# Kernel tuning notes

Measured on AMD Instinct MI355X. Metric: run time of the kernel, lower is better.

The kernel has to match this reference:

```python
import jax, jax.numpy as jnp
import numpy as np

BATCH = 4096
DIM = 2048
TEMPERATURE = 0.5


def setup_inputs() -> dict:
    key = jax.random.key(0)
    k1, k2 = jax.random.split(key)
    c_i = jax.random.normal(k1, (BATCH, DIM), dtype=jnp.float32)
    c_j = jax.random.normal(k2, (BATCH, DIM), dtype=jnp.float32)
    return {"c_i": c_i, "c_j": c_j}


def reference(c_i, c_j):
    # Original torch loop computes, for each i,j:
    #   kl[i, j] = sum_k softmax(c_j[j])_k * (log_softmax(c_j[j])_k - log_softmax(c_i[i])_k)
    #   logits = -kl / T ; loss = CE(logits, arange(B), reduction='sum') / B
    # Fused: kl = hneg[None, :] - Li @ Q.T where hneg[j] = sum_k Q[j]*logQ[j].
    B = c_i.shape[0]
    Li = jax.nn.log_softmax(c_i, axis=-1)          # [B, D]
    LQ = jax.nn.log_softmax(c_j, axis=-1)          # [B, D]
    Q = jnp.exp(LQ)                                # softmax(c_j)
    hneg = jnp.sum(Q * LQ, axis=-1)                # [B] negative entropy of each c_j row
    cross = jnp.einsum("id,jd->ij", Li, Q)         # [B, B] sum_k Li[i,k]*Q[j,k]
    kl = hneg[None, :] - cross                     # [B, B]
    logits = -kl / TEMPERATURE
    logp = jax.nn.log_softmax(logits, axis=-1)     # [B, B]
    loss = -jnp.sum(jnp.diagonal(logp)) / B        # CE(sum) / batch_size
    return loss
```

## Files before the change

### kernel.cpp

```cpp
#include <hip/hip_runtime.h>
#include <hip/hip_bf16.h>
#include <math.h>

#define BATCH 4096
#define DIM   2048
#define INV_T 2.0f

#define BM 128
#define BN 128

typedef float floatx4 __attribute__((ext_vector_type(4)));
typedef int   intx4   __attribute__((ext_vector_type(4)));
typedef int   intx8   __attribute__((ext_vector_type(8)));

static __device__ __forceinline__ void gld_lds16(const void* g, void* l) {
  __builtin_amdgcn_global_load_lds(
      (const __attribute__((address_space(1))) void*)g,
      (__attribute__((address_space(3))) void*)l, 16, 0, 0);
}

static __device__ __forceinline__ intx8 comb8(intx4 lo, intx4 hi) {
  intx8 r;
  r[0] = lo[0]; r[1] = lo[1]; r[2] = lo[2]; r[3] = lo[3];
  r[4] = hi[0]; r[5] = hi[1]; r[6] = hi[2]; r[7] = hi[3];
  return r;
}

__global__ __launch_bounds__(256) void prep_kernel(
    const float* __restrict__ ci, const float* __restrict__ cj,
    unsigned char* __restrict__ Li8, unsigned char* __restrict__ Qb8,
    float* __restrict__ hneg, float* __restrict__ isc,
    float* __restrict__ rowsum, float* __restrict__ out)
{
  const int lane = threadIdx.x & 63;
  const int wave = threadIdx.x >> 6;
  const int row = blockIdx.x * 4 + wave;
  const bool isj = row >= BATCH;
  const int r = isj ? row - BATCH : row;
  const float* __restrict__ src = (isj ? cj : ci) + (size_t)r * DIM;

  float v[32];
  #pragma unroll
  for (int i = 0; i < 8; ++i) {
    float4 t = ((const float4*)src)[i * 64 + lane];
    v[i * 4 + 0] = t.x; v[i * 4 + 1] = t.y;
    v[i * 4 + 2] = t.z; v[i * 4 + 3] = t.w;
  }

  float m = v[0];
  #pragma unroll
  for (int i = 1; i < 32; ++i) m = fmaxf(m, v[i]);
  #pragma unroll
  for (int off = 32; off >= 1; off >>= 1) m = fmaxf(m, __shfl_xor(m, off));

  float s = 0.f;
  #pragma unroll
  for (int i = 0; i < 32; ++i) s += __expf(v[i] - m);
  #pragma unroll
  for (int off = 32; off >= 1; off >>= 1) s += __shfl_xor(s, off);
  const float ls = m + __logf(s);

  float scale = 1.f;
  int t = 0;
  if (isj) {
    const float qmax = __expf(m - ls);
    const int be = (int)((__float_as_uint(qmax) >> 23) & 0xff);
    t = 134 - be;
    scale = __uint_as_float((unsigned)(t + 127) << 23);
  }

  unsigned char* dst = (isj ? Qb8 : Li8) + (size_t)r * DIM;
  float h = 0.f;
  #pragma unroll
  for (int i = 0; i < 8; ++i) {
    float f[4];
    #pragma unroll
    for (int j = 0; j < 4; ++j) {
      const float li = v[i * 4 + j] - ls;
      if (isj) {
        const float q = __expf(li);
        h += q * li;
        f[j] = q * scale;
      } else {
        f[j] = li;
      }
    }
    int w = __builtin_amdgcn_cvt_pk_fp8_f32(f[0], f[1], 0, false);
    w = __builtin_amdgcn_cvt_pk_fp8_f32(f[2], f[3], w, true);
    ((int*)dst)[i * 64 + lane] = w;
  }

  if (isj) {
    #pragma unroll
    for (int off = 32; off >= 1; off >>= 1) h += __shfl_xor(h, off);
    if (lane == 0) {
      hneg[r] = h;
      isc[r] = __uint_as_float((unsigned)(127 - t) << 23);
      rowsum[r] = 0.f;
    }
  }
  if (row == 0 && lane == 0) out[0] = 0.f;
}

__global__ __launch_bounds__(256, 3) void gemm_lse_kernel(
    const unsigned char* __restrict__ Li8, const unsigned char* __restrict__ Qb8,
    const float* __restrict__ hneg, const float* __restrict__ isc,
    float* __restrict__ rowsum, float* __restrict__ diag)
{
  __shared__ __attribute__((aligned(16))) unsigned char As[BM * 128];
  __shared__ __attribute__((aligned(16))) unsigned char Bs[BN * 128];

  const int tid  = threadIdx.x;
  const int lin = blockIdx.x;
  const int xc  = lin & 7;
  const int sq  = lin >> 3;
  const int bx  = (xc << 2) | (sq & 3);
  const int by  = sq >> 2;
  const int lane = tid & 63;
  const int wave = tid >> 6;
  const int wm   = (wave >> 1) * 64;
  const int wn   = (wave & 1) * 64;

  int soff[4];
  #pragma unroll
  for (int s = 0; s < 4; ++s) {
    const int p = tid + 256 * s;
    const int row = p >> 3;
    const int cbg = (p & 7) ^ (row & 7);
    soff[s] = row * DIM + cbg * 16;
  }
  const unsigned char* Abase = Li8 + (size_t)(by * BM) * DIM;
  const unsigned char* Bbase = Qb8 + (size_t)(bx * BN) * DIM;

  const int rl = lane & 15;
  const int q  = lane >> 4;
  const int sw = rl & 7;

  floatx4 acc[4][4];
  const floatx4 z = {0.f, 0.f, 0.f, 0.f};
  #pragma unroll
  for (int mt = 0; mt < 4; ++mt)
    #pragma unroll
    for (int nt = 0; nt < 4; ++nt) acc[mt][nt] = z;

  for (int k = 0; k < DIM; k += 128) {
    #pragma unroll
    for (int s = 0; s < 4; ++s) {
      gld_lds16(Abase + soff[s] + k, As + (tid + 256 * s) * 16);
      gld_lds16(Bbase + soff[s] + k, Bs + (tid + 256 * s) * 16);
    }
    __syncthreads();

    intx8 bf[4];
    #pragma unroll
    for (int t = 0; t < 4; ++t) {
      const int rb = wn + t * 16 + rl;
      const int q0 = rb * 8 + ((2 * q) ^ sw);
      const int q1 = rb * 8 + ((2 * q + 1) ^ sw);
      bf[t] = comb8(*(const intx4*)(Bs + q0 * 16), *(const intx4*)(Bs + q1 * 16));
    }
    #pragma unroll
    for (int mt = 0; mt < 4; ++mt) {
      const int ra = wm + mt * 16 + rl;
      const int p0 = ra * 8 + ((2 * q) ^ sw);
      const int p1 = ra * 8 + ((2 * q + 1) ^ sw);
      const intx8 af = comb8(*(const intx4*)(As + p0 * 16),
                             *(const intx4*)(As + p1 * 16));
      #pragma unroll
      for (int nt = 0; nt < 4; ++nt)
        acc[mt][nt] = __builtin_amdgcn_mfma_scale_f32_16x16x128_f8f6f4(
            af, bf[nt], acc[mt][nt],
            0, 0,
            0, 127,
            0, 127);
    }
    __syncthreads();
  }

  const int col0 = bx * BN + wn + rl;
  float hn[4], sc[4];
  #pragma unroll
  for (int nt = 0; nt < 4; ++nt) {
    hn[nt] = hneg[col0 + nt * 16];
    sc[nt] = isc[col0 + nt * 16];
  }
  const int row0 = by * BM + wm + (q << 2);

  if (bx == by && wm == wn && q == (rl >> 2)) {
    #pragma unroll
    for (int mt = 0; mt < 4; ++mt)
      diag[by * BM + wm + mt * 16 + rl] = acc[mt][mt][rl & 3] * sc[mt];
  }

  #pragma unroll
  for (int mt = 0; mt < 4; ++mt) {
    #pragma unroll
    for (int rr = 0; rr < 4; ++rr) {
      float p = 0.f;
      #pragma unroll
      for (int nt = 0; nt < 4; ++nt)
        p += __expf(INV_T * (acc[mt][nt][rr] * sc[nt] - hn[nt]));
      p += __shfl_xor(p, 1);
      p += __shfl_xor(p, 2);
      p += __shfl_xor(p, 4);
      p += __shfl_xor(p, 8);
      if (rl == 0)
        atomicAdd(&rowsum[row0 + mt * 16 + rr], p);
    }
  }
}

__global__ __launch_bounds__(256) void finalize_kernel(
    const float* __restrict__ hneg, const float* __restrict__ rowsum,
    const float* __restrict__ diag, float* __restrict__ out)
{
  const int i = blockIdx.x * 256 + threadIdx.x;
  const int lane = threadIdx.x & 63;
  const int wave = threadIdx.x >> 6;

  float c = __logf(rowsum[i]) - INV_T * (diag[i] - hneg[i]);
  #pragma unroll
  for (int off = 32; off >= 1; off >>= 1) c += __shfl_xor(c, off);

  __shared__ float red[4];
  if (lane == 0) red[wave] = c;
  __syncthreads();
  if (threadIdx.x == 0)
    atomicAdd(out, (red[0] + red[1] + red[2] + red[3]) * (1.0f / BATCH));
}

extern "C" void kernel_launch(void* const* d_in, const int* in_sizes, int n_in,
                              void* d_out, int out_size, void* d_ws, size_t ws_size,
                              hipStream_t stream) {
  const float* ci = (const float*)d_in[0];
  const float* cj = (const float*)d_in[1];
  float* out = (float*)d_out;

  unsigned char* Li8 = (unsigned char*)d_ws;
  unsigned char* Qb8 = Li8 + (size_t)BATCH * DIM;
  float* hneg   = (float*)(Qb8 + (size_t)BATCH * DIM);
  float* isc    = hneg + BATCH;
  float* rowsum = isc + BATCH;
  float* diag   = rowsum + BATCH;

  prep_kernel<<<2 * BATCH / 4, 256, 0, stream>>>(ci, cj, Li8, Qb8, hneg, isc, rowsum, out);
  gemm_lse_kernel<<<(BATCH / BM) * (BATCH / BN), 256, 0, stream>>>(Li8, Qb8, hneg, isc, rowsum, diag);
  finalize_kernel<<<BATCH / 256, 256, 0, stream>>>(hneg, rowsum, diag, out);
}
```

Measured before the change: 148.6 us.

## Enlarge GEMM tiles to 256x256 with double-buffered LDS prefetch pipeline

Grows the block tile from 128x128 to 256x256 with 512 threads (8 waves, each computing 128x64). LDS is double-buffered so the next K-slice's global-to-LDS loads are issued in phases and overlap the MFMAs, with manual waitcnt/barriers and setprio around the MFMA bursts. This is meant to cut global traffic per FLOP and hide load latency. In exchange it raises LDS use to 128KB per block and register pressure, which lowers occupancy, and leaves only 256 blocks for the grid.

```diff
diff --git a/kernel.cpp b/kernel.cpp
--- a/kernel.cpp
+++ b/kernel.cpp
@@ -6,8 +6,8 @@
 #define DIM   2048
 #define INV_T 2.0f
 
-#define BM 128
-#define BN 128
+#define BM 256
+#define BN 256
 
 typedef float floatx4 __attribute__((ext_vector_type(4)));
 typedef int   intx4   __attribute__((ext_vector_type(4)));
@@ -102,29 +102,30 @@
   if (row == 0 && lane == 0) out[0] = 0.f;
 }
 
-__global__ __launch_bounds__(256, 3) void gemm_lse_kernel(
+__global__ __launch_bounds__(512, 2) void gemm_lse_kernel(
     const unsigned char* __restrict__ Li8, const unsigned char* __restrict__ Qb8,
     const float* __restrict__ hneg, const float* __restrict__ isc,
     float* __restrict__ rowsum, float* __restrict__ diag)
 {
-  __shared__ __attribute__((aligned(16))) unsigned char As[BM * 128];
-  __shared__ __attribute__((aligned(16))) unsigned char Bs[BN * 128];
+  __shared__ __attribute__((aligned(16))) unsigned char As_[2][BM * 128];
+  __shared__ __attribute__((aligned(16))) unsigned char Bs_[2][BN * 128];
 
   const int tid  = threadIdx.x;
   const int lin = blockIdx.x;
   const int xc  = lin & 7;
   const int sq  = lin >> 3;
-  const int bx  = (xc << 2) | (sq & 3);
-  const int by  = sq >> 2;
+  const int by  = (xc & 3) * 4 + (sq & 3);
+  const int bx  = (xc >> 2) * 8 + (sq >> 2);
+
   const int lane = tid & 63;
   const int wave = tid >> 6;
-  const int wm   = (wave >> 1) * 64;
-  const int wn   = (wave & 1) * 64;
+  const int wm   = wave >> 2;
+  const int wn   = wave & 3;
 
   int soff[4];
   #pragma unroll
   for (int s = 0; s < 4; ++s) {
-    const int p = tid + 256 * s;
+    const int p = tid + 512 * s;
     const int row = p >> 3;
     const int cbg = (p & 7) ^ (row & 7);
     soff[s] = row * DIM + cbg * 16;
@@ -136,64 +137,106 @@
   const int q  = lane >> 4;
   const int sw = rl & 7;
 
-  floatx4 acc[4][4];
+  floatx4 acc[8][4];
   const floatx4 z = {0.f, 0.f, 0.f, 0.f};
   #pragma unroll
-  for (int mt = 0; mt < 4; ++mt)
+  for (int mt = 0; mt < 8; ++mt)
     #pragma unroll
     for (int nt = 0; nt < 4; ++nt) acc[mt][nt] = z;
 
-  for (int k = 0; k < DIM; k += 128) {
-    #pragma unroll
-    for (int s = 0; s < 4; ++s) {
-      gld_lds16(Abase + soff[s] + k, As + (tid + 256 * s) * 16);
-      gld_lds16(Bbase + soff[s] + k, Bs + (tid + 256 * s) * 16);
-    }
-    __syncthreads();
+  #pragma unroll
+  for (int s = 0; s < 4; ++s) {
+    gld_lds16(Abase + soff[s], &As_[0][0] + (tid + 512 * s) * 16);
+    gld_lds16(Bbase + soff[s], &Bs_[0][0] + (tid + 512 * s) * 16);
+  }
+
+  for (int t = 0; t < 16; ++t) {
+    const unsigned char* Ab = &As_[t & 1][0];
+    const unsigned char* Bb = &Bs_[t & 1][0];
+    unsigned char* An = &As_[(t & 1) ^ 1][0];
+    unsigned char* Bn = &Bs_[(t & 1) ^ 1][0];
+    const int kn = (t + 1) * 128;
+    const bool pf = (t < 15);
 
     intx8 bf[4];
-    #pragma unroll
-    for (int t = 0; t < 4; ++t) {
-      const int rb = wn + t * 16 + rl;
-      const int q0 = rb * 8 + ((2 * q) ^ sw);
-      const int q1 = rb * 8 + ((2 * q + 1) ^ sw);
-      bf[t] = comb8(*(const intx4*)(Bs + q0 * 16), *(const intx4*)(Bs + q1 * 16));
-    }
-    #pragma unroll
-    for (int mt = 0; mt < 4; ++mt) {
-      const int ra = wm + mt * 16 + rl;
-      const int p0 = ra * 8 + ((2 * q) ^ sw);
-      const int p1 = ra * 8 + ((2 * q + 1) ^ sw);
-      const intx8 af = comb8(*(const intx4*)(As + p0 * 16),
-                             *(const intx4*)(As + p1 * 16));
+
+    #pragma unroll
+    for (int p = 0; p < 4; ++p) {
+      if (p == 0) {
+        if (pf) {
+          gld_lds16(Abase + soff[0] + kn, An + tid * 16);
+          gld_lds16(Bbase + soff[0] + kn, Bn + tid * 16);
+          asm volatile("s_waitcnt vmcnt(2)" ::: "memory");
+        } else {
+          asm volatile("s_waitcnt vmcnt(0)" ::: "memory");
+        }
+        asm volatile("s_barrier" ::: "memory");
+        #pragma unroll
+        for (int nt = 0; nt < 4; ++nt) {
+          const int rb = wn * 64 + nt * 16 + rl;
+          const int q0 = rb * 8 + ((2 * q) ^ sw);
+          const int q1 = rb * 8 + ((2 * q + 1) ^ sw);
+          bf[nt] = comb8(*(const intx4*)(Bb + q0 * 16),
+                         *(const intx4*)(Bb + q1 * 16));
+        }
+      }
+      intx8 af0, af1;
+      {
+        const int ra0 = wm * 128 + (2 * p) * 16 + rl;
+        const int a00 = ra0 * 8 + ((2 * q) ^ sw);
+        const int a01 = ra0 * 8 + ((2 * q + 1) ^ sw);
+        af0 = comb8(*(const intx4*)(Ab + a00 * 16),
+                    *(const intx4*)(Ab + a01 * 16));
+        const int ra1 = wm * 128 + (2 * p + 1) * 16 + rl;
+        const int a10 = ra1 * 8 + ((2 * q) ^ sw);
+        const int a11 = ra1 * 8 + ((2 * q + 1) ^ sw);
+        af1 = comb8(*(const intx4*)(Ab + a10 * 16),
+                    *(const intx4*)(Ab + a11 * 16));
+      }
+      if (p != 0) {
+        if (pf) {
+          gld_lds16(Abase + soff[p] + kn, An + (tid + 512 * p) * 16);
+          gld_lds16(Bbase + soff[p] + kn, Bn + (tid + 512 * p) * 16);
+        }
+        asm volatile("s_barrier" ::: "memory");
+      }
+      __builtin_amdgcn_s_setprio(1);
       #pragma unroll
       for (int nt = 0; nt < 4; ++nt)
-        acc[mt][nt] = __builtin_amdgcn_mfma_scale_f32_16x16x128_f8f6f4(
-            af, bf[nt], acc[mt][nt],
+        acc[2 * p + 0][nt] = __builtin_amdgcn_mfma_scale_f32_16x16x128_f8f6f4(
+            af0, bf[nt], acc[2 * p + 0][nt],
             0, 0,
             0, 127,
             0, 127);
-    }
-    __syncthreads();
-  }
-
-  const int col0 = bx * BN + wn + rl;
+      #pragma unroll
+      for (int nt = 0; nt < 4; ++nt)
+        acc[2 * p + 1][nt] = __builtin_amdgcn_mfma_scale_f32_16x16x128_f8f6f4(
+            af1, bf[nt], acc[2 * p + 1][nt],
+            0, 0, 0, 127, 0, 127);
+      __builtin_amdgcn_s_setprio(0);
+      asm volatile("s_barrier" ::: "memory");
+    }
+  }
+
+  const int col0 = bx * BN + wn * 64 + rl;
   float hn[4], sc[4];
   #pragma unroll
   for (int nt = 0; nt < 4; ++nt) {
     hn[nt] = hneg[col0 + nt * 16];
     sc[nt] = isc[col0 + nt * 16];
   }
-  const int row0 = by * BM + wm + (q << 2);
-
-  if (bx == by && wm == wn && q == (rl >> 2)) {
-    #pragma unroll
-    for (int mt = 0; mt < 4; ++mt)
-      diag[by * BM + wm + mt * 16 + rl] = acc[mt][mt][rl & 3] * sc[mt];
-  }
-
-  #pragma unroll
-  for (int mt = 0; mt < 4; ++mt) {
+  const int row0 = by * BM + wm * 128 + (q << 2);
+
+  if (bx == by && wm == (wn >> 1) && q == (rl >> 2)) {
+    #pragma unroll
+    for (int nt = 0; nt < 4; ++nt) {
+      const int mt = (wn & 1) * 4 + nt;
+      diag[bx * BN + wn * 64 + nt * 16 + rl] = acc[mt][nt][rl & 3] * sc[nt];
+    }
+  }
+
+  #pragma unroll
+  for (int mt = 0; mt < 8; ++mt) {
     #pragma unroll
     for (int rr = 0; rr < 4; ++rr) {
       float p = 0.f;
@@ -244,6 +287,6 @@
   float* diag   = rowsum + BATCH;
 
   prep_kernel<<<2 * BATCH / 4, 256, 0, stream>>>(ci, cj, Li8, Qb8, hneg, isc, rowsum, out);
-  gemm_lse_kernel<<<(BATCH / BM) * (BATCH / BN), 256, 0, stream>>>(Li8, Qb8, hneg, isc, rowsum, diag);
+  gemm_lse_kernel<<<(BATCH / BM) * (BATCH / BN), 512, 0, stream>>>(Li8, Qb8, hneg, isc, rowsum, diag);
   finalize_kernel<<<BATCH / 256, 256, 0, stream>>>(hneg, rowsum, diag, out);
 }
```

Result: slower. 169.3 us (+13.9%).
